# Kernel optimization log

Measured on AMD Instinct MI355X. Metric: run time of the kernel, lower is better.

## Reference

```python
import jax, jax.numpy as jnp
import numpy as np

B, L, V, E, H = 64, 512, 256, 512, 1024


def setup_inputs() -> dict:
    key = jax.random.key(0)
    ks = jax.random.split(key, 6)
    s = lambda n: 1.0 / np.sqrt(n)
    return {
        "x": jax.random.randint(ks[0], (B, L), 0, V),
        "emb": jax.random.normal(ks[1], (V, E), jnp.float32),
        "U_w": jax.random.normal(ks[2], (H, E), jnp.float32) * s(E),
        "V_w": jax.random.normal(ks[3], (H, H), jnp.float32) * s(H),
        "alpha": jnp.ones((H,), jnp.float32),
        "beta1": jnp.ones((H,), jnp.float32),
        "beta2": jnp.ones((H,), jnp.float32),
        "bias": jnp.zeros((H,), jnp.float32),
        "dec_w": jax.random.normal(ks[4], (V, H), jnp.float32) * s(H),
        "dec_b": jnp.zeros((V,), jnp.float32),
    }


def reference(x, emb, U_w, V_w, alpha, beta1, beta2, bias, dec_w, dec_b):
    e = emb[x]                                   # [B, L, E]
    # Precompute input projection for all timesteps (U has no bias)
    Ux = jnp.einsum("ble,he->blh", e, U_w)       # [B, L, H]
    h0 = jnp.zeros((x.shape[0], V_w.shape[0]), e.dtype)

    def step(h, ux_t):
        Vh = h @ V_w.T                           # [B, H]
        m = alpha * (Vh * ux_t) + beta1 * Vh + beta2 * ux_t + bias
        h_new = jnp.tanh(m)
        return h_new, h_new

    h_last, hs = jax.lax.scan(step, h0, jnp.swapaxes(Ux, 0, 1))  # hs: [L, B, H]
    out = jnp.swapaxes(hs, 0, 1)                 # [B, L, H]
    logits = jnp.einsum("blh,vh->blv", out, dec_w) + dec_b
    return logits, h_last[None, :, :]
```

## Files before the change

kernel.cpp:

```cpp
#include <hip/hip_runtime.h>

#define DI __device__ __forceinline__

typedef short s16x4 __attribute__((ext_vector_type(4)));
typedef short s16x8 __attribute__((ext_vector_type(8)));
typedef float f32x4 __attribute__((ext_vector_type(4)));

constexpr int CB = 64, CL = 512, CV = 256, CE = 512, CH = 1024;
constexpr int CBL = CB * CL;
constexpr size_t LOGN = (size_t)CBL * CV;
constexpr unsigned SLOT = (unsigned)CB * CH * 2;

constexpr size_t WS_BAR   = 0;
constexpr size_t WS_XCDT  = 1024;
constexpr size_t WS_RING  = 4096;
constexpr size_t WS_EMBB  = WS_RING + 2u*SLOT;
constexpr size_t WS_UWB   = WS_EMBB + (size_t)CV*CE*2;
constexpr size_t WS_VWB   = WS_UWB  + (size_t)CH*CE*2;
constexpr size_t WS_DECWB = WS_VWB  + (size_t)CH*CH*2;
constexpr size_t WS_UX    = WS_DECWB+ (size_t)CV*CH*2;
constexpr size_t WS_HS    = WS_UX   + (size_t)CBL*CH*2;

DI unsigned short f2bf(float f) {
  unsigned u = __float_as_uint(f);
  u += 0x7FFFu + ((u >> 16) & 1u);
  return (unsigned short)(u >> 16);
}
DI float bf2f(unsigned short h) { return __uint_as_float(((unsigned)h) << 16); }

DI f32x4 mfma_bf16(s16x8 a, s16x8 b, f32x4 c) {
  return __builtin_amdgcn_mfma_f32_16x16x32_bf16(a, b, c, 0, 0, 0);
}

DI float fast_tanh(float x) {
  float a = fminf(fabsf(x), 20.0f);
  float e = __expf(-2.0f * a);
  float r = (1.0f - e) / (1.0f + e);
  return __builtin_copysignf(r, x);
}

__global__ __launch_bounds__(256) void k_convert(
    const float* __restrict__ emb, const float* __restrict__ uw,
    const float* __restrict__ vw,  const float* __restrict__ dw,
    unsigned short* __restrict__ embb, unsigned short* __restrict__ uwb,
    unsigned short* __restrict__ vwb,  unsigned short* __restrict__ dwb)
{
  int i = (blockIdx.x * 256 + threadIdx.x) * 4;
  const float* s; unsigned short* d; int off;
  if      (i < 131072)  { s = emb; d = embb; off = i; }
  else if (i < 655360)  { s = uw;  d = uwb;  off = i - 131072; }
  else if (i < 1703936) { s = vw;  d = vwb;  off = i - 655360; }
  else                  { s = dw;  d = dwb;  off = i - 1703936; }
  float4 v = *(const float4*)(s + off);
  ushort4 o; o.x = f2bf(v.x); o.y = f2bf(v.y); o.z = f2bf(v.z); o.w = f2bf(v.w);
  *(ushort4*)(d + off) = o;
}

template<int KD, int NT, bool GATHER, bool OUTF32>
__global__ __launch_bounds__(256) void k_gemm(
    const unsigned short* __restrict__ Asrc,
    const int* __restrict__ xidx,
    const unsigned short* __restrict__ Bsrc,
    const float* __restrict__ biasv,
    unsigned short* __restrict__ Cb,
    float* __restrict__ Cf)
{
  __shared__ unsigned char As[64 * 128];
  __shared__ unsigned char Bs[64 * 128];
  __shared__ int xs[64];

  const int tid = threadIdx.x;
  const int rt = blockIdx.x, ct = blockIdx.y;
  const int r0 = rt * 64, c0 = ct * 64;

  if (GATHER) {
    if (tid < 64) xs[tid] = xidx[r0 + tid];
    __syncthreads();
  }

  const int r  = tid >> 2, kq = tid & 3;
  const unsigned short* aRow = GATHER ? (Asrc + (size_t)xs[r] * KD)
                                      : (Asrc + (size_t)(r0 + r) * KD);
  const unsigned short* bRow = Bsrc + (size_t)(c0 + r) * KD;
  const int dstOff = r * 128 + ((kq * 16) ^ ((r & 7) << 4));

  const int wave = tid >> 6, lane = tid & 63;
  const int ln15 = lane & 15, lg = lane >> 4;
  const int xr = (lane & 7) << 4;
  int aOff[4];
#pragma unroll
  for (int m = 0; m < 4; ++m) aOff[m] = (m * 16 + ln15) * 128 + ((lg * 16) ^ xr);
  const int bOff = (wave * 16 + ln15) * 128 + ((lg * 16) ^ xr);

  f32x4 acc[4] = {};
  for (int kk = 0; kk < KD / 32; ++kk) {
    s16x8 av = *(const s16x8*)(aRow + kk * 32 + kq * 8);
    s16x8 bv = *(const s16x8*)(bRow + kk * 32 + kq * 8);
    __syncthreads();
    *(s16x8*)(As + dstOff) = av;
    *(s16x8*)(Bs + dstOff) = bv;
    __syncthreads();
    s16x8 bf = *(const s16x8*)(Bs + bOff);
#pragma unroll
    for (int m = 0; m < 4; ++m) {
      s16x8 af = *(const s16x8*)(As + aOff[m]);
      acc[m] = mfma_bf16(af, bf, acc[m]);
    }
  }

  const int colg = c0 + wave * 16 + ln15;
  float bv = 0.f;
  if (OUTF32) bv = biasv[colg];
#pragma unroll
  for (int m = 0; m < 4; ++m) {
#pragma unroll
    for (int rr = 0; rr < 4; ++rr) {
      int rowg = r0 + m * 16 + lg * 4 + rr;
      if (OUTF32) Cf[(size_t)rowg * NT + colg] = acc[m][rr] + bv;
      else        Cb[(size_t)rowg * NT + colg] = f2bf(acc[m][rr]);
    }
  }
}

struct FastTag { static constexpr bool fast = true;  };
struct SafeTag { static constexpr bool fast = false; };

__global__ __launch_bounds__(512, 1) void k_rec(
    const unsigned short* __restrict__ vwb,
    const unsigned short* __restrict__ ux,
    unsigned short* __restrict__ ring,
    unsigned short* __restrict__ hs,
    const float* __restrict__ alpha, const float* __restrict__ beta1,
    const float* __restrict__ beta2, const float* __restrict__ bias,
    float* __restrict__ out, int* flags, int* xcdtab)
{
  __shared__ __align__(16) unsigned char hlds[2][16 * 2048];
  __shared__ int smode;

  const int bid = blockIdx.x;
  const int bg = bid & 7, cs = bid >> 3;
  if (bg >= 4) return;
  const int tid = threadIdx.x;
  const int wave = tid >> 6, lane = tid & 63;
  const int ln15 = lane & 15, lg = lane >> 4;
  const int b0 = bg * 16;
  const int colbase = cs * 128 + wave * 16 + lg * 4;
  const int myb = b0 + ln15;

  int* gxt = xcdtab + bg * 16;
  if (tid == 0) {
    unsigned myxcd;
    asm volatile("s_getreg_b32 %0, hwreg(HW_REG_XCC_ID)" : "=s"(myxcd));
    myxcd &= 15u;
    __hip_atomic_store(&gxt[cs], (int)myxcd, __ATOMIC_RELAXED, __HIP_MEMORY_SCOPE_SYSTEM);
    int first = -1; bool same = true;
    for (int i = 0; i < 8;) {
      int v = __hip_atomic_load(&gxt[i], __ATOMIC_RELAXED, __HIP_MEMORY_SCOPE_SYSTEM);
      if (v == -1) { __builtin_amdgcn_s_sleep(8); continue; }
      if (first == -1) first = v; else if (v != first) same = false;
      ++i;
    }
    smode = same ? 1 : 0;
  }
  __syncthreads();
  const bool fastmode = (smode != 0);

  s16x8 breg[32];
  {
    const unsigned short* vrow = vwb + (size_t)(cs * 128 + wave * 16 + ln15) * CH + lg * 8;
#pragma unroll
    for (int kc = 0; kc < 32; ++kc) breg[kc] = *(const s16x8*)(vrow + kc * 32);
  }
#pragma unroll
  for (int kc = 0; kc < 32; ++kc) asm volatile("" : "+v"(breg[kc]));

  const float4 alv = *(const float4*)(alpha + colbase);
  const float4 b1v = *(const float4*)(beta1 + colbase);
  const float4 b2v = *(const float4*)(beta2 + colbase);
  const float4 biv = *(const float4*)(bias  + colbase);

  __amdgpu_buffer_rsrc_t rsrd = __builtin_amdgcn_make_buffer_rsrc(
      (void*)ring, (short)0, (int)(2u * SLOT), 0x00020000);

  int* gflags = flags + bg * 64;
  const int myflag = cs * 8 + wave;

  int sRow[4], sCol[4];
#pragma unroll
  for (int i = 0; i < 4; ++i) {
    const int L = i * 8192 + tid * 16;
    sRow[i] = L >> 11;
    sCol[i] = (L & 2047) ^ ((sRow[i] & 15) << 4);
  }
  const unsigned stgBase = (unsigned)(b0 * 2048);

  const int fBase = ln15 * 2048;
  const int fXor  = ln15 << 4;
  const unsigned cellOff = (unsigned)(myb * 2048 + colbase * 2);

  s16x4 uxv = *(const s16x4*)(ux + ((size_t)myb * CL + 0) * CH + colbase);

  auto run = [&](auto tag) {
    constexpr int  AUX = decltype(tag)::fast ? 1 : 17;
    constexpr auto SCP = decltype(tag)::fast ? __HIP_MEMORY_SCOPE_AGENT
                                             : __HIP_MEMORY_SCOPE_SYSTEM;
    for (int t = 0; t < CL; ++t) {
      f32x4 vh = {};
      if (t > 0) {
        bool ok;
        do {
          int fv = __hip_atomic_load(&gflags[lane], __ATOMIC_RELAXED, SCP);
          ok = __all(fv >= t) != 0;
        } while (!ok);
        asm volatile("" ::: "memory");

        const unsigned roff = ((unsigned)((t - 1) & 1)) * SLOT + stgBase;
        s16x8 stg[4];
#pragma unroll
        for (int i = 0; i < 4; ++i) {
          auto raw = __builtin_amdgcn_raw_buffer_load_b128(
              rsrd, (int)(roff + i * 8192 + tid * 16), 0, AUX);
          stg[i] = __builtin_bit_cast(s16x8, raw);
        }
        unsigned char* lb = hlds[t & 1];
#pragma unroll
        for (int i = 0; i < 4; ++i)
          *(s16x8*)(lb + sRow[i] * 2048 + sCol[i]) = stg[i];
        __syncthreads();

        f32x4 a0 = {}, a1 = {}, a2 = {}, a3 = {};
#pragma unroll
        for (int kc = 0; kc < 32; kc += 4) {
          s16x8 f0 = *(const s16x8*)(lb + fBase + ((lg * 16 + kc * 64)       ^ fXor));
          s16x8 f1 = *(const s16x8*)(lb + fBase + ((lg * 16 + kc * 64 + 64)  ^ fXor));
          s16x8 f2 = *(const s16x8*)(lb + fBase + ((lg * 16 + kc * 64 + 128) ^ fXor));
          s16x8 f3 = *(const s16x8*)(lb + fBase + ((lg * 16 + kc * 64 + 192) ^ fXor));
          a0 = mfma_bf16(breg[kc],     f0, a0);
          a1 = mfma_bf16(breg[kc + 1], f1, a1);
          a2 = mfma_bf16(breg[kc + 2], f2, a2);
          a3 = mfma_bf16(breg[kc + 3], f3, a3);
        }
        vh = (a0 + a1) + (a2 + a3);
      }

      float hnv[4]; unsigned short hbv[4];
#pragma unroll
      for (int rr = 0; rr < 4; ++rr) {
        const float u = bf2f((unsigned short)uxv[rr]);
        const float v = vh[rr];
        const float mm = (&alv.x)[rr] * (v * u) + (&b1v.x)[rr] * v +
                         (&b2v.x)[rr] * u + (&biv.x)[rr];
        hnv[rr] = fast_tanh(mm);
        hbv[rr] = f2bf(hnv[rr]);
      }

      const unsigned long long pk = (unsigned long long)hbv[0]
                                  | ((unsigned long long)hbv[1] << 16)
                                  | ((unsigned long long)hbv[2] << 32)
                                  | ((unsigned long long)hbv[3] << 48);

      if (t < CL - 1) {
        unsigned long long* hp = (unsigned long long*)
            ((char*)ring + (size_t)(t & 1) * SLOT + cellOff);
        __hip_atomic_store(hp, pk, __ATOMIC_RELAXED, SCP);
        asm volatile("s_waitcnt vmcnt(0)" ::: "memory");
        if (lane == 0)
          __hip_atomic_store(&gflags[myflag], t + 1, __ATOMIC_RELAXED, SCP);
        *(unsigned long long*)(hs + ((size_t)myb * CL + t) * CH + colbase) = pk;
        uxv = *(const s16x4*)(ux + ((size_t)myb * CL + (t + 1)) * CH + colbase);
      } else {
        *(unsigned long long*)(hs + ((size_t)myb * CL + t) * CH + colbase) = pk;
        float4 o; o.x = hnv[0]; o.y = hnv[1]; o.z = hnv[2]; o.w = hnv[3];
        *(float4*)(out + LOGN + (size_t)myb * CH + colbase) = o;
      }
    }
  };
  if (fastmode) run(FastTag{}); else run(SafeTag{});
}

extern "C" void kernel_launch(void* const* d_in, const int* in_sizes, int n_in,
                              void* d_out, int out_size, void* d_ws, size_t ws_size,
                              hipStream_t stream) {
  const int*   x     = (const int*)  d_in[0];
  const float* emb   = (const float*)d_in[1];
  const float* Uw    = (const float*)d_in[2];
  const float* Vw    = (const float*)d_in[3];
  const float* alpha = (const float*)d_in[4];
  const float* beta1 = (const float*)d_in[5];
  const float* beta2 = (const float*)d_in[6];
  const float* bias  = (const float*)d_in[7];
  const float* decw  = (const float*)d_in[8];
  const float* decb  = (const float*)d_in[9];
  float* out = (float*)d_out;
  char*  ws  = (char*)d_ws;

  int*            flags = (int*)(ws + WS_BAR);
  int*            xcdt  = (int*)(ws + WS_XCDT);
  unsigned short* ring  = (unsigned short*)(ws + WS_RING);
  unsigned short* embb  = (unsigned short*)(ws + WS_EMBB);
  unsigned short* uwb   = (unsigned short*)(ws + WS_UWB);
  unsigned short* vwb   = (unsigned short*)(ws + WS_VWB);
  unsigned short* dwb   = (unsigned short*)(ws + WS_DECWB);
  unsigned short* uxb   = (unsigned short*)(ws + WS_UX);
  unsigned short* hsb   = (unsigned short*)(ws + WS_HS);

  (void)hipMemsetAsync(ws + WS_BAR, 0, 1024, stream);
  (void)hipMemsetAsync(ws + WS_XCDT, 0xFF, 256, stream);

  k_convert<<<1920, 256, 0, stream>>>(emb, Uw, Vw, decw, embb, uwb, vwb, dwb);

  k_gemm<CE, CH, true, false><<<dim3(CBL / 64, CH / 64), 256, 0, stream>>>(
      embb, x, uwb, nullptr, uxb, nullptr);

  k_rec<<<64, 512, 0, stream>>>(vwb, uxb, ring, hsb, alpha, beta1, beta2, bias,
                                out, flags, xcdt);

  k_gemm<CH, CV, false, true><<<dim3(CBL / 64, CV / 64), 256, 0, stream>>>(
      hsb, nullptr, dwb, decb, nullptr, out);
}
```

Measured before the change: 1.546 ms.

## Enlarge GEMM tiles to 128x128 with 4x4 MFMA per wave and padded LDS

The input-projection and decoder GEMMs move from 64x64 tiles, where each wave computed a 64x16 strip, to 128x128 tiles with a 2x2 wave grid. Each wave now computes 64x64 with 16 accumulators, so every LDS fragment is reused across four MFMAs. The XOR swizzle is replaced by a padded pitch of 40 elements. This cuts global and LDS traffic per FLOP, at the cost of more registers and fewer blocks; the recurrence kernel, which likely dominates total time, is unchanged.

```diff
diff --git a/kernel.cpp b/kernel.cpp
--- a/kernel.cpp
+++ b/kernel.cpp
@@ -65,59 +65,75 @@
     unsigned short* __restrict__ Cb,
     float* __restrict__ Cf)
 {
-  __shared__ unsigned char As[64 * 128];
-  __shared__ unsigned char Bs[64 * 128];
-  __shared__ int xs[64];
+  constexpr int PITCH = 40;
+  __shared__ unsigned short As[128 * PITCH];
+  __shared__ unsigned short Bs[128 * PITCH];
+  __shared__ int xs[128];
 
   const int tid = threadIdx.x;
-  const int rt = blockIdx.x, ct = blockIdx.y;
-  const int r0 = rt * 64, c0 = ct * 64;
+  const int r0 = blockIdx.x * 128, c0 = blockIdx.y * 128;
 
   if (GATHER) {
-    if (tid < 64) xs[tid] = xidx[r0 + tid];
+    if (tid < 128) xs[tid] = xidx[r0 + tid];
     __syncthreads();
   }
 
-  const int r  = tid >> 2, kq = tid & 3;
-  const unsigned short* aRow = GATHER ? (Asrc + (size_t)xs[r] * KD)
-                                      : (Asrc + (size_t)(r0 + r) * KD);
-  const unsigned short* bRow = Bsrc + (size_t)(c0 + r) * KD;
-  const int dstOff = r * 128 + ((kq * 16) ^ ((r & 7) << 4));
+  const int sr = tid >> 1, ss = (tid & 1) * 16;
+  const unsigned short* aRow =
+      (GATHER ? (Asrc + (size_t)xs[sr] * KD) : (Asrc + (size_t)(r0 + sr) * KD)) + ss;
+  const unsigned short* bRow = Bsrc + (size_t)(c0 + sr) * KD + ss;
+  unsigned short* aDst = As + sr * PITCH + ss;
+  unsigned short* bDst = Bs + sr * PITCH + ss;
 
   const int wave = tid >> 6, lane = tid & 63;
   const int ln15 = lane & 15, lg = lane >> 4;
-  const int xr = (lane & 7) << 4;
-  int aOff[4];
-#pragma unroll
-  for (int m = 0; m < 4; ++m) aOff[m] = (m * 16 + ln15) * 128 + ((lg * 16) ^ xr);
-  const int bOff = (wave * 16 + ln15) * 128 + ((lg * 16) ^ xr);
-
-  f32x4 acc[4] = {};
+  const int wm = wave >> 1, wn = wave & 1;
+
+  int aOff[4], bOff[4];
+#pragma unroll
+  for (int m = 0; m < 4; ++m) aOff[m] = (wm * 64 + m * 16 + ln15) * PITCH + lg * 8;
+#pragma unroll
+  for (int n = 0; n < 4; ++n) bOff[n] = (wn * 64 + n * 16 + ln15) * PITCH + lg * 8;
+
+  f32x4 acc[4][4] = {};
+
   for (int kk = 0; kk < KD / 32; ++kk) {
-    s16x8 av = *(const s16x8*)(aRow + kk * 32 + kq * 8);
-    s16x8 bv = *(const s16x8*)(bRow + kk * 32 + kq * 8);
+    s16x8 av0 = *(const s16x8*)(aRow + kk * 32);
+    s16x8 av1 = *(const s16x8*)(aRow + kk * 32 + 8);
+    s16x8 bv0 = *(const s16x8*)(bRow + kk * 32);
+    s16x8 bv1 = *(const s16x8*)(bRow + kk * 32 + 8);
     __syncthreads();
-    *(s16x8*)(As + dstOff) = av;
-    *(s16x8*)(Bs + dstOff) = bv;
+    *(s16x8*)(aDst)     = av0;
+    *(s16x8*)(aDst + 8) = av1;
+    *(s16x8*)(bDst)     = bv0;
+    *(s16x8*)(bDst + 8) = bv1;
     __syncthreads();
-    s16x8 bf = *(const s16x8*)(Bs + bOff);
+
+    s16x8 bf[4];
+#pragma unroll
+    for (int n = 0; n < 4; ++n) bf[n] = *(const s16x8*)(Bs + bOff[n]);
 #pragma unroll
     for (int m = 0; m < 4; ++m) {
       s16x8 af = *(const s16x8*)(As + aOff[m]);
-      acc[m] = mfma_bf16(af, bf, acc[m]);
+#pragma unroll
+      for (int n = 0; n < 4; ++n)
+        acc[m][n] = mfma_bf16(af, bf[n], acc[m][n]);
     }
   }
 
-  const int colg = c0 + wave * 16 + ln15;
-  float bv = 0.f;
-  if (OUTF32) bv = biasv[colg];
 #pragma unroll
   for (int m = 0; m < 4; ++m) {
 #pragma unroll
-    for (int rr = 0; rr < 4; ++rr) {
-      int rowg = r0 + m * 16 + lg * 4 + rr;
-      if (OUTF32) Cf[(size_t)rowg * NT + colg] = acc[m][rr] + bv;
-      else        Cb[(size_t)rowg * NT + colg] = f2bf(acc[m][rr]);
+    for (int n = 0; n < 4; ++n) {
+      const int colg = c0 + wn * 64 + n * 16 + ln15;
+      float bv = 0.f;
+      if (OUTF32) bv = biasv[colg];
+#pragma unroll
+      for (int rr = 0; rr < 4; ++rr) {
+        const int rowg = r0 + wm * 64 + m * 16 + lg * 4 + rr;
+        if (OUTF32) Cf[(size_t)rowg * NT + colg] = acc[m][n][rr] + bv;
+        else        Cb[(size_t)rowg * NT + colg] = f2bf(acc[m][n][rr]);
+      }
     }
   }
 }
@@ -309,12 +325,12 @@
 
   k_convert<<<1920, 256, 0, stream>>>(emb, Uw, Vw, decw, embb, uwb, vwb, dwb);
 
-  k_gemm<CE, CH, true, false><<<dim3(CBL / 64, CH / 64), 256, 0, stream>>>(
+  k_gemm<CE, CH, true, false><<<dim3(CBL / 128, CH / 128), 256, 0, stream>>>(
       embb, x, uwb, nullptr, uxb, nullptr);
 
   k_rec<<<64, 512, 0, stream>>>(vwb, uxb, ring, hsb, alpha, beta1, beta2, bias,
                                 out, flags, xcdt);
 
-  k_gemm<CH, CV, false, true><<<dim3(CBL / 64, CV / 64), 256, 0, stream>>>(
+  k_gemm<CH, CV, false, true><<<dim3(CBL / 128, CV / 128), 256, 0, stream>>>(
       hsb, nullptr, dwb, decb, nullptr, out);
 }
```

Measured after the change: 1.422 ms. 8.1% less time.
